# Performance work log

Hardware: AMD Instinct MI355X
Metric: run time of the kernel (lower is better)

## Reference

```python
import jax, jax.numpy as jnp
import numpy as np
import math

EPS = 1e-5

def _ln(x, g, b):
    m = jnp.mean(x, axis=-1, keepdims=True)
    v = jnp.var(x, axis=-1, keepdims=True)
    return (x - m) * jax.lax.rsqrt(v + EPS) * g + b

def _rn_layer(x, W, g, b, A, Bb, Rw):
    # x: (B,S,in) -> (B,S,out). W: (out,in), A: (out,basis), Bb: (basis,out)
    S = x.shape[1]
    basis_dim = Bb.shape[0]
    n = _ln(x @ W.T, g, b)                      # (B,S,out)
    j = jnp.arange(S) % basis_dim               # (S,)
    Bv = Bb[j]                                  # (S,out)
    scal = jnp.einsum('bsd,sd->bs', n, Bv)      # (B,S)
    Av = A[:, j].T                              # (S,out)
    nf = scal[..., None] * Av                   # (B,S,out)
    res = x if Rw is None else x @ Rw.T
    return nf + res

def _ts_layer(x, M, g, b, P, Rw):
    # x: (B,S,in) -> (B,S,out). M: (out,in), P: (out,out,G)
    S = x.shape[1]
    D, _, G = P.shape
    t = _ln(x @ M.T, g, b)                      # (B,S,out)
    k = jnp.arange(S, dtype=jnp.float32)
    periods = (jnp.arange(D, dtype=jnp.float32)[:, None, None] * (D * G)
               + jnp.arange(D, dtype=jnp.float32)[None, :, None] * G
               + jnp.arange(G, dtype=jnp.float32)[None, None, :] + 2.0)  # (D,D,G)
    phi = jnp.cos(2.0 * math.pi * k[:, None, None, None] / periods)       # (S,D,D,G)
    # Nk[b,s,i] = sum_{j,g} P[i,j,g] * t[b,s,j] * phi[s,i,j,g]
    Wp = jnp.einsum('ijg,sijg->sij', P, phi)    # (S,D,D)
    Nk = jnp.einsum('sij,bsj->bsi', Wp, t)      # (B,S,D)
    return Nk + x @ Rw.T

def setup_inputs() -> dict:
    key = jax.random.key(0)
    ks = jax.random.split(key, 16)
    B, S = 2, 2048
    d0, d1, d2 = 512, 64, 512        # input_dim, ts out, final out
    bas1, G, bas3 = 64, 8, 64
    u = lambda k, sh, a: jax.random.uniform(k, sh, jnp.float32, -a, a)
    inp = {
        'x':  jax.random.normal(ks[0], (B, S, d0), jnp.float32),
        # Layer 1: RN 512->512 (in==out -> no residual proj)
        'W1': u(ks[1], (d0, d0), 0.1),
        'g1': jnp.ones((d0,), jnp.float32),
        'b1': jnp.zeros((d0,), jnp.float32),
        'A1': u(ks[2], (d0, bas1), 0.1),
        'B1': u(ks[3], (bas1, d0), 0.1),
        # Layer 2: TS 512->64
        'M2': u(ks[4], (d1, d0), 0.5),
        'g2': jnp.ones((d1,), jnp.float32),
        'b2': jnp.zeros((d1,), jnp.float32),
        'P2': u(ks[5], (d1, d1, G), 0.1),
        'R2': u(ks[6], (d1, d0), 0.1),
        # Layer 3: RN 64->512
        'W3': u(ks[7], (d2, d1), 0.1),
        'g3': jnp.ones((d2,), jnp.float32),
        'b3': jnp.zeros((d2,), jnp.float32),
        'A3': u(ks[8], (d2, bas3), 0.1),
        'B3': u(ks[9], (bas3, d2), 0.1),
        'R3': u(ks[10], (d2, d1), 0.1),
    }
    return inp

def reference(x, W1, g1, b1, A1, B1, M2, g2, b2, P2, R2, W3, g3, b3, A3, B3, R3):
    h = _rn_layer(x, W1, g1, b1, A1, B1, None)   # (B,S,512), identity residual
    h = _ts_layer(h, M2, g2, b2, P2, R2)         # (B,S,64)
    h = _rn_layer(h, W3, g3, b3, A3, B3, R3)     # (B,S,512)
    return h
```

## Files before the change

kernel.cpp:

```cpp
#include <hip/hip_runtime.h>
#include <math.h>

#define SEQ  2048
#define ROWS 4096
#define D0   512
#define D1   64

typedef short bf8 __attribute__((ext_vector_type(8)));
typedef float f4  __attribute__((ext_vector_type(4)));

__device__ __forceinline__ unsigned short f2bf(float f) {
    unsigned u = __float_as_uint(f);
    return (unsigned short)((u + 0x7fffu + ((u >> 16) & 1u)) >> 16);
}
__device__ __forceinline__ void hilo(float f, unsigned short& h, unsigned short& l) {
    h = f2bf(f);
    float fh = __uint_as_float((unsigned)h << 16);
    l = f2bf(f - fh);
}
__device__ __forceinline__ void cv4(unsigned short* dh, unsigned short* dl, int idx, float4 v) {
    ushort4 hv, lv;
    hilo(v.x, hv.x, lv.x); hilo(v.y, hv.y, lv.y);
    hilo(v.z, hv.z, lv.z); hilo(v.w, hv.w, lv.w);
    *(ushort4*)(dh + idx) = hv;
    *(ushort4*)(dl + idx) = lv;
}
__device__ __forceinline__ void cv4h(unsigned short* dh, int idx, float4 v) {
    ushort4 hv;
    hv.x = f2bf(v.x); hv.y = f2bf(v.y); hv.z = f2bf(v.z); hv.w = f2bf(v.w);
    *(ushort4*)(dh + idx) = hv;
}

__device__ __forceinline__ void async16(const void* g, void* l) {
    __builtin_amdgcn_global_load_lds(
        (const __attribute__((address_space(1))) unsigned int*)g,
        (__attribute__((address_space(3))) unsigned int*)l, 16, 0, 0);
}

__global__ __launch_bounds__(256) void convk(
        const float* __restrict__ x,  const float* __restrict__ W1,
        const float* __restrict__ M2, const float* __restrict__ R2,
        const float* __restrict__ W3, const float* __restrict__ R3,
        const float* __restrict__ A1, const float* __restrict__ A3,
        unsigned short* __restrict__ xh,  unsigned short* __restrict__ xl,
        unsigned short* __restrict__ W1h,
        unsigned short* __restrict__ C2h,
        unsigned short* __restrict__ C3h,
        float* __restrict__ A1T, float* __restrict__ A3T) {
    int c = blockIdx.x, tid = threadIdx.x;
    if (c < 1024) {
        int base = c * 2048 + tid * 4;
        cv4(xh, xl, base,        *(const float4*)(x + base));
        cv4(xh, xl, base + 1024, *(const float4*)(x + base + 1024));
    } else if (c < 1216) {
        const float* src; unsigned short* dh; int off;
        if      (c < 1152) { src = W1; dh = W1h;         off = c - 1024; }
        else if (c < 1168) { src = M2; dh = C2h;         off = c - 1152; }
        else if (c < 1184) { src = R2; dh = C2h + 32768; off = c - 1168; }
        else if (c < 1200) { src = W3; dh = C3h;         off = c - 1184; }
        else               { src = R3; dh = C3h + 32768; off = c - 1200; }
        int base = off * 2048 + tid * 4;
        cv4h(dh, base,        *(const float4*)(src + base));
        cv4h(dh, base + 1024, *(const float4*)(src + base + 1024));
    } else {
        int gid = (c - 1216) * 256 + tid;
        int i = gid >> 6, j = gid & 63;
        A1T[j * 512 + i] = A1[gid];
        A3T[j * 512 + i] = A3[gid];
    }
}

__global__ __launch_bounds__(256, 4) void gemm128(
        const unsigned short* __restrict__ Ah, const unsigned short* __restrict__ Al,
        const unsigned short* __restrict__ Wh,
        float* __restrict__ C, int M, int N, int K, int Ks) {
    __shared__ __align__(16) unsigned short aH[8192], aL[8192], wH[4096];
    const int tid = threadIdx.x;
    const int wv  = tid >> 6;
    const int ln  = tid & 63;
    const int lm  = ln & 15;
    const int lq  = ln >> 4;
    const int bm  = blockIdx.y * 128;
    const int bn  = blockIdx.x * 64;
    const int k0  = blockIdx.z * Ks;
    C += (size_t)blockIdx.z * M * N;

    f4 acc[2][4] = {};

    for (int kt = 0; kt < Ks; kt += 64) {
        const int kg = k0 + kt;
        __syncthreads();
#pragma unroll
        for (int i = 0; i < 4; ++i) {
            int slot = i * 256 + wv * 64 + ln;
            int row  = slot >> 3;
            int ch   = (slot & 7) ^ (row & 7);
            size_t go = (size_t)(bm + row) * K + kg + ch * 8;
            async16(Ah + go, aH + slot * 8);
            async16(Al + go, aL + slot * 8);
        }
#pragma unroll
        for (int i = 0; i < 2; ++i) {
            int slot = i * 256 + wv * 64 + ln;
            int row  = slot >> 3;
            int ch   = (slot & 7) ^ (row & 7);
            size_t go = (size_t)(bn + row) * K + kg + ch * 8;
            async16(Wh + go, wH + slot * 8);
        }
        __syncthreads();

#pragma unroll
        for (int kk = 0; kk < 2; ++kk) {
            const int ck = kk * 4 + lq;
            bf8 a_h[2], a_l[2], b_h[4];
#pragma unroll
            for (int t = 0; t < 2; ++t) {
                int r = wv * 32 + t * 16 + lm;
                a_h[t] = *(const bf8*)(aH + r * 64 + ((ck ^ (r & 7)) * 8));
                a_l[t] = *(const bf8*)(aL + r * 64 + ((ck ^ (r & 7)) * 8));
            }
#pragma unroll
            for (int u = 0; u < 4; ++u) {
                int rb = u * 16 + lm;
                b_h[u] = *(const bf8*)(wH + rb * 64 + ((ck ^ (rb & 7)) * 8));
            }
#pragma unroll
            for (int t = 0; t < 2; ++t)
#pragma unroll
                for (int u = 0; u < 4; ++u) {
                    acc[t][u] = __builtin_amdgcn_mfma_f32_16x16x32_bf16(a_h[t], b_h[u], acc[t][u], 0, 0, 0);
                    acc[t][u] = __builtin_amdgcn_mfma_f32_16x16x32_bf16(a_l[t], b_h[u], acc[t][u], 0, 0, 0);
                }
        }
    }

#pragma unroll
    for (int t = 0; t < 2; ++t)
#pragma unroll
        for (int u = 0; u < 4; ++u) {
            int row = bm + wv * 32 + t * 16 + lq * 4;
            int col = bn + u * 16 + lm;
#pragma unroll
            for (int r = 0; r < 4; ++r)
                C[(size_t)(row + r) * N + col] = acc[t][u][r];
        }
}

__global__ __launch_bounds__(256) void lnrn(
        const float* __restrict__ Y, const float* __restrict__ Y2, int ldy,
        const float* __restrict__ RES, int ldr,
        const float* __restrict__ g, const float* __restrict__ be,
        const float* __restrict__ Bb, const float* __restrict__ AaT,
        float* __restrict__ outf,
        unsigned short* __restrict__ outh, unsigned short* __restrict__ outl) {
    const int row = blockIdx.x * 4 + (threadIdx.x >> 6);
    const int l = threadIdx.x & 63;
    const int c = l * 8;
    const float* y = Y + (size_t)row * ldy + c;
    float4 y0 = *(const float4*)y;
    float4 y1 = *(const float4*)(y + 4);
    if (Y2) {
        const float* y2 = Y2 + (size_t)row * ldy + c;
        float4 p0 = *(const float4*)y2, p1 = *(const float4*)(y2 + 4);
        y0.x += p0.x; y0.y += p0.y; y0.z += p0.z; y0.w += p0.w;
        y1.x += p1.x; y1.y += p1.y; y1.z += p1.z; y1.w += p1.w;
    }
    float sum = y0.x + y0.y + y0.z + y0.w + y1.x + y1.y + y1.z + y1.w;
    float ssq = y0.x*y0.x + y0.y*y0.y + y0.z*y0.z + y0.w*y0.w
              + y1.x*y1.x + y1.y*y1.y + y1.z*y1.z + y1.w*y1.w;
#pragma unroll
    for (int m = 1; m < 64; m <<= 1) {
        sum += __shfl_xor(sum, m, 64);
        ssq += __shfl_xor(ssq, m, 64);
    }
    float mean = sum * (1.0f / 512.0f);
    float var  = ssq * (1.0f / 512.0f) - mean * mean;
    float rstd = rsqrtf(var + 1e-5f);
    float4 g0 = *(const float4*)(g + c),  g1v = *(const float4*)(g + c + 4);
    float4 e0 = *(const float4*)(be + c), e1  = *(const float4*)(be + c + 4);
    float4 n0, n1;
    n0.x = (y0.x - mean) * rstd * g0.x  + e0.x;
    n0.y = (y0.y - mean) * rstd * g0.y  + e0.y;
    n0.z = (y0.z - mean) * rstd * g0.z  + e0.z;
    n0.w = (y0.w - mean) * rstd * g0.w  + e0.w;
    n1.x = (y1.x - mean) * rstd * g1v.x + e1.x;
    n1.y = (y1.y - mean) * rstd * g1v.y + e1.y;
    n1.z = (y1.z - mean) * rstd * g1v.z + e1.z;
    n1.w = (y1.w - mean) * rstd * g1v.w + e1.w;
    const int jm = row & 63;
    const float* bb = Bb + jm * D0 + c;
    float4 b0 = *(const float4*)bb, b1v = *(const float4*)(bb + 4);
    float p = n0.x*b0.x + n0.y*b0.y + n0.z*b0.z + n0.w*b0.w
            + n1.x*b1v.x + n1.y*b1v.y + n1.z*b1v.z + n1.w*b1v.w;
#pragma unroll
    for (int m = 1; m < 64; m <<= 1) p += __shfl_xor(p, m, 64);
    const float* av = AaT + jm * D0 + c;
    float4 a0 = *(const float4*)av, a1 = *(const float4*)(av + 4);
    const float* rs = RES + (size_t)row * ldr + c;
    float4 r0 = *(const float4*)rs, r1 = *(const float4*)(rs + 4);
    float4 v0, v1;
    v0.x = p*a0.x + r0.x; v0.y = p*a0.y + r0.y; v0.z = p*a0.z + r0.z; v0.w = p*a0.w + r0.w;
    v1.x = p*a1.x + r1.x; v1.y = p*a1.y + r1.y; v1.z = p*a1.z + r1.z; v1.w = p*a1.w + r1.w;
    if (outf) {
        *(float4*)(outf + (size_t)row * D0 + c)     = v0;
        *(float4*)(outf + (size_t)row * D0 + c + 4) = v1;
    } else {
        ushort4 h0, l0, h1, l1;
        hilo(v0.x, h0.x, l0.x); hilo(v0.y, h0.y, l0.y);
        hilo(v0.z, h0.z, l0.z); hilo(v0.w, h0.w, l0.w);
        hilo(v1.x, h1.x, l1.x); hilo(v1.y, h1.y, l1.y);
        hilo(v1.z, h1.z, l1.z); hilo(v1.w, h1.w, l1.w);
        *(ushort4*)(outh + (size_t)row * D0 + c)     = h0;
        *(ushort4*)(outl + (size_t)row * D0 + c)     = l0;
        *(ushort4*)(outh + (size_t)row * D0 + c + 4) = h1;
        *(ushort4*)(outl + (size_t)row * D0 + c + 4) = l1;
    }
}

#define C2S 524288
__global__ __launch_bounds__(256) void lnt(
        const float* __restrict__ C2, const float* __restrict__ g2,
        const float* __restrict__ b2,
        float* __restrict__ t, float* __restrict__ rsum) {
    const int r = blockIdx.x * 4 + (threadIdx.x >> 6);
    const int j = threadIdx.x & 63;
    size_t base = (size_t)r * 128 + j;
    float v = 0.f, rv = 0.f;
#pragma unroll
    for (int z = 0; z < 4; ++z) {
        v  += C2[(size_t)z * C2S + base];
        rv += C2[(size_t)z * C2S + base + 64];
    }
    float sum = v, ssq = v * v;
#pragma unroll
    for (int m = 1; m < 64; m <<= 1) {
        sum += __shfl_xor(sum, m, 64);
        ssq += __shfl_xor(ssq, m, 64);
    }
    float mean = sum * (1.0f / 64.0f);
    float var  = ssq * (1.0f / 64.0f) - mean * mean;
    float rstd = rsqrtf(var + 1e-5f);
    t[r * 64 + j]    = (v - mean) * rstd * g2[j] + b2[j];
    rsum[r * 64 + j] = rv;
}

__global__ __launch_bounds__(256) void tsk2(
        const float* __restrict__ t, const float* __restrict__ rsum,
        const float* __restrict__ P,
        unsigned short* __restrict__ Hh, unsigned short* __restrict__ Hl) {
    const int bid = blockIdx.x;
    const int i   = bid >> 3;
    const int sg  = bid & 7;
    const int w   = threadIdx.x >> 6;
    const int ln  = threadIdx.x & 63;
    const int s0  = sg * 256 + w * 64;
    const int idx = i * 64 + ln;
    const float* pp = P + idx * 8;
    const float sf0 = (float)s0;

    float k2c[8], ca[8], cb[8];
#pragma unroll
    for (int g = 0; g < 8; ++g) {
        float pf   = (float)(idx * 8 + g + 2);
        float invp = __builtin_amdgcn_rcpf(pf);
        k2c[g] = 2.0f * __builtin_amdgcn_cosf(invp);
        float q0 = floorf(sf0 * invp);
        float r0 = fmaf(-q0, pf, sf0);
        float f0 = r0 * invp; f0 -= floorf(f0);
        float c0 = __builtin_amdgcn_cosf(f0);
        float sf1 = sf0 + 1.0f;
        float q1 = floorf(sf1 * invp);
        float r1 = fmaf(-q1, pf, sf1);
        float f1 = r1 * invp; f1 -= floorf(f1);
        float c1 = __builtin_amdgcn_cosf(f1);
        float Pv = pp[g];
        ca[g] = Pv * c0;
        cb[g] = Pv * c1;
    }

    const int tb = s0 * 64 + ln;
    float t0c = t[tb], t1c = t[131072 + tb];
    float res0 = 0.f, res1 = 0.f;

    for (int st = 0; st < 64; st += 2) {
        float t0n  = t[tb + (st + 1) * 64];
        float t1n  = t[131072 + tb + (st + 1) * 64];
        float ws = ((ca[0] + ca[1]) + (ca[2] + ca[3]))
                 + ((ca[4] + ca[5]) + (ca[6] + ca[7]));
#pragma unroll
        for (int g = 0; g < 8; ++g) ca[g] = fmaf(k2c[g], cb[g], -ca[g]);
        float v0 = ws * t0c, v1 = ws * t1c;
#pragma unroll
        for (int m = 1; m < 64; m <<= 1) {
            v0 += __shfl_xor(v0, m, 64);
            v1 += __shfl_xor(v1, m, 64);
        }
        res0 = (ln == st) ? v0 : res0;
        res1 = (ln == st) ? v1 : res1;
        float t0n2 = t[tb + (st + 2) * 64];
        float t1n2 = t[131072 + tb + (st + 2) * 64];
        float ws2 = ((cb[0] + cb[1]) + (cb[2] + cb[3]))
                  + ((cb[4] + cb[5]) + (cb[6] + cb[7]));
#pragma unroll
        for (int g = 0; g < 8; ++g) cb[g] = fmaf(k2c[g], ca[g], -cb[g]);
        float v0b = ws2 * t0n, v1b = ws2 * t1n;
#pragma unroll
        for (int m = 1; m < 64; m <<= 1) {
            v0b += __shfl_xor(v0b, m, 64);
            v1b += __shfl_xor(v1b, m, 64);
        }
        res0 = (ln == st + 1) ? v0b : res0;
        res1 = (ln == st + 1) ? v1b : res1;
        t0c = t0n2; t1c = t1n2;
    }

    const int s = s0 + ln;
    {
        float v = res0 + rsum[(size_t)s * 64 + i];
        unsigned short h, l; hilo(v, h, l);
        Hh[(size_t)s * 64 + i] = h; Hl[(size_t)s * 64 + i] = l;
        float v1e = res1 + rsum[(size_t)(SEQ + s) * 64 + i];
        hilo(v1e, h, l);
        Hh[(size_t)(SEQ + s) * 64 + i] = h; Hl[(size_t)(SEQ + s) * 64 + i] = l;
    }
}

extern "C" void kernel_launch(void* const* d_in, const int* in_sizes, int n_in,
                              void* d_out, int out_size, void* d_ws, size_t ws_size,
                              hipStream_t stream) {
    const float* x  = (const float*)d_in[0];
    const float* W1 = (const float*)d_in[1];
    const float* g1 = (const float*)d_in[2];
    const float* b1 = (const float*)d_in[3];
    const float* A1 = (const float*)d_in[4];
    const float* B1 = (const float*)d_in[5];
    const float* M2 = (const float*)d_in[6];
    const float* g2 = (const float*)d_in[7];
    const float* b2 = (const float*)d_in[8];
    const float* P2 = (const float*)d_in[9];
    const float* R2 = (const float*)d_in[10];
    const float* W3 = (const float*)d_in[11];
    const float* g3 = (const float*)d_in[12];
    const float* b3 = (const float*)d_in[13];
    const float* A3 = (const float*)d_in[14];
    const float* B3 = (const float*)d_in[15];
    const float* R3 = (const float*)d_in[16];

    float* ws = (float*)d_ws;
    float* C1   = ws;
    float* C2   = ws + 4194304;
    float* C3   = ws + 6291456;
    float* t    = ws + 10485760;
    float* rsum = ws + 10747904;
    float* A1T  = ws + 11010048;
    float* A3T  = ws + 11042816;
    unsigned short* us = (unsigned short*)(ws + 11075584);
    unsigned short* xh   = us;
    unsigned short* xl   = us + 2097152;
    unsigned short* h1h  = us + 4194304;
    unsigned short* h1l  = us + 6291456;
    unsigned short* W1h  = us + 8388608;
    unsigned short* Wc2h = us + 8650752;
    unsigned short* Wc3h = us + 8716288;
    unsigned short* h2h  = us + 8781824;
    unsigned short* h2l  = us + 9043968;

    dim3 blk(256);

    convk<<<1344, blk, 0, stream>>>(x, W1, M2, R2, W3, R3, A1, A3,
                                    xh, xl, W1h, Wc2h, Wc3h, A1T, A3T);

    gemm128<<<dim3(8, 32, 2), blk, 0, stream>>>(xh, xl, W1h, C1, ROWS, 512, 512, 256);
    lnrn<<<1024, blk, 0, stream>>>(C1, C1 + 2097152, 512, x, 512, g1, b1, B1, A1T,
                                   nullptr, h1h, h1l);

    gemm128<<<dim3(2, 32, 4), blk, 0, stream>>>(h1h, h1l, Wc2h, C2, ROWS, 128, 512, 128);
    lnt<<<1024, blk, 0, stream>>>(C2, g2, b2, t, rsum);
    tsk2<<<512, blk, 0, stream>>>(t, rsum, P2, h2h, h2l);

    gemm128<<<dim3(16, 32, 1), blk, 0, stream>>>(h2h, h2l, Wc3h, C3, ROWS, 1024, 64, 64);
    lnrn<<<1024, blk, 0, stream>>>(C3, nullptr, 1024, C3 + 512, 1024, g3, b3, B3, A3T,
                                   (float*)d_out, nullptr, nullptr);
}
```

Baseline: 160.7 us.

## Drop x low-part split and store pre-LN GEMM outputs as bf16

The layer-1 GEMM now runs on the bf16 high part of x only, with no low-part correction pass, which removes half of its MFMAs and A-tile loads. The layer-1 pre-layernorm split-K partials and the layer-3 pre-layernorm output are written as bf16 instead of fp32, which shrinks intermediate traffic and workspace. The layer-3 residual part stays fp32. The cost is lower precision in the pre-layernorm values, which may affect accuracy after normalization.

```diff
diff --git a/kernel.cpp b/kernel.cpp
--- a/kernel.cpp
+++ b/kernel.cpp
@@ -13,17 +13,13 @@
     unsigned u = __float_as_uint(f);
     return (unsigned short)((u + 0x7fffu + ((u >> 16) & 1u)) >> 16);
 }
+__device__ __forceinline__ float bf2f(unsigned short u) {
+    return __uint_as_float((unsigned)u << 16);
+}
 __device__ __forceinline__ void hilo(float f, unsigned short& h, unsigned short& l) {
     h = f2bf(f);
-    float fh = __uint_as_float((unsigned)h << 16);
+    float fh = bf2f(h);
     l = f2bf(f - fh);
-}
-__device__ __forceinline__ void cv4(unsigned short* dh, unsigned short* dl, int idx, float4 v) {
-    ushort4 hv, lv;
-    hilo(v.x, hv.x, lv.x); hilo(v.y, hv.y, lv.y);
-    hilo(v.z, hv.z, lv.z); hilo(v.w, hv.w, lv.w);
-    *(ushort4*)(dh + idx) = hv;
-    *(ushort4*)(dl + idx) = lv;
 }
 __device__ __forceinline__ void cv4h(unsigned short* dh, int idx, float4 v) {
     ushort4 hv;
@@ -42,19 +38,16 @@
         const float* __restrict__ M2, const float* __restrict__ R2,
         const float* __restrict__ W3, const float* __restrict__ R3,
         const float* __restrict__ A1, const float* __restrict__ A3,
-        unsigned short* __restrict__ xh,  unsigned short* __restrict__ xl,
+        unsigned short* __restrict__ xh,
         unsigned short* __restrict__ W1h,
         unsigned short* __restrict__ C2h,
         unsigned short* __restrict__ C3h,
         float* __restrict__ A1T, float* __restrict__ A3T) {
     int c = blockIdx.x, tid = threadIdx.x;
-    if (c < 1024) {
-        int base = c * 2048 + tid * 4;
-        cv4(xh, xl, base,        *(const float4*)(x + base));
-        cv4(xh, xl, base + 1024, *(const float4*)(x + base + 1024));
-    } else if (c < 1216) {
+    if (c < 1216) {
         const float* src; unsigned short* dh; int off;
-        if      (c < 1152) { src = W1; dh = W1h;         off = c - 1024; }
+        if      (c < 1024) { src = x;  dh = xh;          off = c; }
+        else if (c < 1152) { src = W1; dh = W1h;         off = c - 1024; }
         else if (c < 1168) { src = M2; dh = C2h;         off = c - 1152; }
         else if (c < 1184) { src = R2; dh = C2h + 32768; off = c - 1168; }
         else if (c < 1200) { src = W3; dh = C3h;         off = c - 1184; }
@@ -70,11 +63,15 @@
     }
 }
 
-__global__ __launch_bounds__(256, 4) void gemm128(
+template<bool ALO, int OM>
+__global__ __launch_bounds__(256, 4) void gemm128t(
         const unsigned short* __restrict__ Ah, const unsigned short* __restrict__ Al,
         const unsigned short* __restrict__ Wh,
-        float* __restrict__ C, int M, int N, int K, int Ks) {
-    __shared__ __align__(16) unsigned short aH[8192], aL[8192], wH[4096];
+        float* __restrict__ Cf, unsigned short* __restrict__ Cb,
+        int M, int N, int K, int Ks) {
+    __shared__ __align__(16) unsigned short aH[8192];
+    __shared__ __align__(16) unsigned short aL[ALO ? 8192 : 16];
+    __shared__ __align__(16) unsigned short wH[4096];
     const int tid = threadIdx.x;
     const int wv  = tid >> 6;
     const int ln  = tid & 63;
@@ -83,7 +80,6 @@
     const int bm  = blockIdx.y * 128;
     const int bn  = blockIdx.x * 64;
     const int k0  = blockIdx.z * Ks;
-    C += (size_t)blockIdx.z * M * N;
 
     f4 acc[2][4] = {};
 
@@ -97,7 +93,7 @@
             int ch   = (slot & 7) ^ (row & 7);
             size_t go = (size_t)(bm + row) * K + kg + ch * 8;
             async16(Ah + go, aH + slot * 8);
-            async16(Al + go, aL + slot * 8);
+            if constexpr (ALO) async16(Al + go, aL + slot * 8);
         }
 #pragma unroll
         for (int i = 0; i < 2; ++i) {
@@ -117,7 +113,8 @@
             for (int t = 0; t < 2; ++t) {
                 int r = wv * 32 + t * 16 + lm;
                 a_h[t] = *(const bf8*)(aH + r * 64 + ((ck ^ (r & 7)) * 8));
-                a_l[t] = *(const bf8*)(aL + r * 64 + ((ck ^ (r & 7)) * 8));
+                if constexpr (ALO)
+                    a_l[t] = *(const bf8*)(aL + r * 64 + ((ck ^ (r & 7)) * 8));
             }
 #pragma unroll
             for (int u = 0; u < 4; ++u) {
@@ -129,7 +126,8 @@
 #pragma unroll
                 for (int u = 0; u < 4; ++u) {
                     acc[t][u] = __builtin_amdgcn_mfma_f32_16x16x32_bf16(a_h[t], b_h[u], acc[t][u], 0, 0, 0);
-                    acc[t][u] = __builtin_amdgcn_mfma_f32_16x16x32_bf16(a_l[t], b_h[u], acc[t][u], 0, 0, 0);
+                    if constexpr (ALO)
+                        acc[t][u] = __builtin_amdgcn_mfma_f32_16x16x32_bf16(a_l[t], b_h[u], acc[t][u], 0, 0, 0);
                 }
         }
     }
@@ -141,14 +139,24 @@
             int row = bm + wv * 32 + t * 16 + lq * 4;
             int col = bn + u * 16 + lm;
 #pragma unroll
-            for (int r = 0; r < 4; ++r)
-                C[(size_t)(row + r) * N + col] = acc[t][u][r];
+            for (int r = 0; r < 4; ++r) {
+                float v = acc[t][u][r];
+                if constexpr (OM == 0) {
+                    Cf[(size_t)blockIdx.z * M * N + (size_t)(row + r) * N + col] = v;
+                } else if constexpr (OM == 1) {
+                    Cb[(size_t)blockIdx.z * M * N + (size_t)(row + r) * N + col] = f2bf(v);
+                } else {
+                    if (col < 512) Cb[(size_t)(row + r) * 512 + col] = f2bf(v);
+                    else           Cf[(size_t)(row + r) * 512 + col - 512] = v;
+                }
+            }
         }
 }
 
 __global__ __launch_bounds__(256) void lnrn(
-        const float* __restrict__ Y, const float* __restrict__ Y2, int ldy,
-        const float* __restrict__ RES, int ldr,
+        const unsigned short* __restrict__ Yb0,
+        const unsigned short* __restrict__ Yb1,
+        const float* __restrict__ RES,
         const float* __restrict__ g, const float* __restrict__ be,
         const float* __restrict__ Bb, const float* __restrict__ AaT,
         float* __restrict__ outf,
@@ -156,14 +164,16 @@
     const int row = blockIdx.x * 4 + (threadIdx.x >> 6);
     const int l = threadIdx.x & 63;
     const int c = l * 8;
-    const float* y = Y + (size_t)row * ldy + c;
-    float4 y0 = *(const float4*)y;
-    float4 y1 = *(const float4*)(y + 4);
-    if (Y2) {
-        const float* y2 = Y2 + (size_t)row * ldy + c;
-        float4 p0 = *(const float4*)y2, p1 = *(const float4*)(y2 + 4);
-        y0.x += p0.x; y0.y += p0.y; y0.z += p0.z; y0.w += p0.w;
-        y1.x += p1.x; y1.y += p1.y; y1.z += p1.z; y1.w += p1.w;
+    ushort4 ua = *(const ushort4*)(Yb0 + (size_t)row * D0 + c);
+    ushort4 ub = *(const ushort4*)(Yb0 + (size_t)row * D0 + c + 4);
+    float4 y0, y1;
+    y0.x = bf2f(ua.x); y0.y = bf2f(ua.y); y0.z = bf2f(ua.z); y0.w = bf2f(ua.w);
+    y1.x = bf2f(ub.x); y1.y = bf2f(ub.y); y1.z = bf2f(ub.z); y1.w = bf2f(ub.w);
+    if (Yb1) {
+        ushort4 va = *(const ushort4*)(Yb1 + (size_t)row * D0 + c);
+        ushort4 vb = *(const ushort4*)(Yb1 + (size_t)row * D0 + c + 4);
+        y0.x += bf2f(va.x); y0.y += bf2f(va.y); y0.z += bf2f(va.z); y0.w += bf2f(va.w);
+        y1.x += bf2f(vb.x); y1.y += bf2f(vb.y); y1.z += bf2f(vb.z); y1.w += bf2f(vb.w);
     }
     float sum = y0.x + y0.y + y0.z + y0.w + y1.x + y1.y + y1.z + y1.w;
     float ssq = y0.x*y0.x + y0.y*y0.y + y0.z*y0.z + y0.w*y0.w
@@ -196,7 +206,7 @@
     for (int m = 1; m < 64; m <<= 1) p += __shfl_xor(p, m, 64);
     const float* av = AaT + jm * D0 + c;
     float4 a0 = *(const float4*)av, a1 = *(const float4*)(av + 4);
-    const float* rs = RES + (size_t)row * ldr + c;
+    const float* rs = RES + (size_t)row * D0 + c;
     float4 r0 = *(const float4*)rs, r1 = *(const float4*)(rs + 4);
     float4 v0, v1;
     v0.x = p*a0.x + r0.x; v0.y = p*a0.y + r0.y; v0.z = p*a0.z + r0.z; v0.w = p*a0.w + r0.w;
@@ -347,38 +357,41 @@
     const float* R3 = (const float*)d_in[16];
 
     float* ws = (float*)d_ws;
-    float* C1   = ws;
-    float* C2   = ws + 4194304;
-    float* C3   = ws + 6291456;
-    float* t    = ws + 10485760;
-    float* rsum = ws + 10747904;
-    float* A1T  = ws + 11010048;
-    float* A3T  = ws + 11042816;
-    unsigned short* us = (unsigned short*)(ws + 11075584);
+    float* C2   = ws;
+    float* C3r  = ws + 2097152;
+    float* t    = ws + 4194304;
+    float* rsum = ws + 4456448;
+    float* A1T  = ws + 4718592;
+    float* A3T  = ws + 4751360;
+    unsigned short* us = (unsigned short*)(ws + 4784128);
     unsigned short* xh   = us;
-    unsigned short* xl   = us + 2097152;
-    unsigned short* h1h  = us + 4194304;
-    unsigned short* h1l  = us + 6291456;
-    unsigned short* W1h  = us + 8388608;
-    unsigned short* Wc2h = us + 8650752;
-    unsigned short* Wc3h = us + 8716288;
-    unsigned short* h2h  = us + 8781824;
-    unsigned short* h2l  = us + 9043968;
+    unsigned short* h1h  = us + 2097152;
+    unsigned short* h1l  = us + 4194304;
+    unsigned short* W1h  = us + 6291456;
+    unsigned short* Wc2h = us + 6553600;
+    unsigned short* Wc3h = us + 6619136;
+    unsigned short* h2h  = us + 6684672;
+    unsigned short* h2l  = us + 6946816;
+    unsigned short* C1b  = us + 7208960;
+    unsigned short* C3n  = us + 11403264;
 
     dim3 blk(256);
 
     convk<<<1344, blk, 0, stream>>>(x, W1, M2, R2, W3, R3, A1, A3,
-                                    xh, xl, W1h, Wc2h, Wc3h, A1T, A3T);
-
-    gemm128<<<dim3(8, 32, 2), blk, 0, stream>>>(xh, xl, W1h, C1, ROWS, 512, 512, 256);
-    lnrn<<<1024, blk, 0, stream>>>(C1, C1 + 2097152, 512, x, 512, g1, b1, B1, A1T,
-                                   nullptr, h1h, h1l);
-
-    gemm128<<<dim3(2, 32, 4), blk, 0, stream>>>(h1h, h1l, Wc2h, C2, ROWS, 128, 512, 128);
+                                    xh, W1h, Wc2h, Wc3h, A1T, A3T);
+
+    gemm128t<false, 1><<<dim3(8, 32, 2), blk, 0, stream>>>(
+        xh, xh, W1h, nullptr, C1b, ROWS, 512, 512, 256);
+    lnrn<<<1024, blk, 0, stream>>>(C1b, C1b + (size_t)ROWS * 512, x,
+                                   g1, b1, B1, A1T, nullptr, h1h, h1l);
+
+    gemm128t<true, 0><<<dim3(2, 32, 4), blk, 0, stream>>>(
+        h1h, h1l, Wc2h, C2, nullptr, ROWS, 128, 512, 128);
     lnt<<<1024, blk, 0, stream>>>(C2, g2, b2, t, rsum);
     tsk2<<<512, blk, 0, stream>>>(t, rsum, P2, h2h, h2l);
 
-    gemm128<<<dim3(16, 32, 1), blk, 0, stream>>>(h2h, h2l, Wc3h, C3, ROWS, 1024, 64, 64);
-    lnrn<<<1024, blk, 0, stream>>>(C3, nullptr, 1024, C3 + 512, 1024, g3, b3, B3, A3T,
+    gemm128t<true, 2><<<dim3(16, 32, 1), blk, 0, stream>>>(
+        h2h, h2l, Wc3h, C3r, C3n, ROWS, 1024, 64, 64);
+    lnrn<<<1024, blk, 0, stream>>>(C3n, nullptr, C3r, g3, b3, B3, A3T,
                                    (float*)d_out, nullptr, nullptr);
 }
```

Result: faster. 151.1 us (-6.0%).
